# Kernel optimization log

Measured on AMD Instinct MI355X. Metric: run time of the kernel, lower is better.

Reference implementation:

```python
import jax, jax.numpy as jnp
import numpy as np

B, S, D = 16, 2048, 64
K, M = 8, 2048

def setup_inputs() -> dict:
    key = jax.random.key(0)
    kx, kc = jax.random.split(key)
    x = jax.random.normal(kx, (B, S, D), dtype=jnp.float32)
    # nn.init.uniform_(weight, -1/M, 1/M)
    codebooks = jax.random.uniform(kc, (K, M, D), dtype=jnp.float32,
                                   minval=-1.0 / M, maxval=1.0 / M)
    return {"x": x, "codebooks": codebooks}

def reference(x, codebooks):
    """Residual VQ: sequentially quantize residual against K codebooks.

    x: (B,S,D) float32; codebooks: (K,M,D) float32.
    Returns (quantized (B,S,D), indices (K,B,S) int32).
    Uses squared-distance expansion ||r||^2 - 2 r.c + ||c||^2 (argmin-equivalent
    to torch.norm) to avoid materializing the (B,S,M,D) difference tensor.
    """
    def step(residual, cb):  # residual: (B,S,D), cb: (M,D)
        r2 = jnp.sum(residual * residual, axis=-1, keepdims=True)   # (B,S,1)
        c2 = jnp.sum(cb * cb, axis=-1)                              # (M,)
        cross = jnp.einsum('bsd,md->bsm', residual, cb)             # (B,S,M)
        d2 = r2 - 2.0 * cross + c2                                  # (B,S,M)
        idx = jnp.argmin(d2, axis=-1)                               # (B,S)
        q = cb[idx]                                                 # (B,S,D) gather
        return residual - q, idx

    residual, indices = jax.lax.scan(step, x, codebooks)
    quantized = x - residual
    return quantized, indices
```

## Files before the change

### kernel.cpp

```cpp
#include <hip/hip_runtime.h>


#define BB 16
#define SS 2048
#define DD 64
#define KK 8
#define MM 2048
#define NPTS (BB * SS)
#define QSIZE (NPTS * DD)
#define WPB 8
#define MCHUNK (MM / WPB)

__global__ __launch_bounds__(256) void rvq_prep(const float* __restrict__ cb,
                                                float* __restrict__ c2) {
#pragma clang fp contract(off)
    int tid = blockIdx.x * 256 + threadIdx.x;
    const float* row = cb + (size_t)tid * DD;
    float r[8];
#pragma unroll
    for (int j = 0; j < 8; ++j) { float v = row[j]; r[j] = v * v; }
#pragma unroll
    for (int i = 8; i < DD; i += 8) {
#pragma unroll
        for (int j = 0; j < 8; ++j) { float v = row[i + j]; float t = v * v; r[j] += t; }
    }
    c2[tid] = ((r[0] + r[1]) + (r[2] + r[3])) + ((r[4] + r[5]) + (r[6] + r[7]));
}

#define R2K(A, B, C, E) \
    "v_pk_mul_f32 v[92:93], v[" A "], v[" A "]\n\t" \
    "v_pk_add_f32 v[80:81], v[80:81], v[92:93]\n\t" \
    "v_pk_mul_f32 v[92:93], v[" B "], v[" B "]\n\t" \
    "v_pk_add_f32 v[82:83], v[82:83], v[92:93]\n\t" \
    "v_pk_mul_f32 v[92:93], v[" C "], v[" C "]\n\t" \
    "v_pk_add_f32 v[84:85], v[84:85], v[92:93]\n\t" \
    "v_pk_mul_f32 v[92:93], v[" E "], v[" E "]\n\t" \
    "v_pk_add_f32 v[86:87], v[86:87], v[92:93]\n\t"

#define GRP(SA, SB, VA, VB) \
    "v_pk_mul_f32 v[84:85], s[" SA "], v[" VA "]\n\t" \
    "v_pk_mul_f32 v[86:87], s[" SB "], v[" VB "]\n\t" \
    "v_pk_add_f32 v[80:81], v[80:81], v[84:85]\n\t" \
    "v_pk_add_f32 v[82:83], v[82:83], v[86:87]\n\t"

__global__ __launch_bounds__(512, 4) void rvq_step(const float* __restrict__ res_in,
                                                   float* __restrict__ res_out,
                                                   const float* __restrict__ cbk,
                                                   const float* __restrict__ c2k,
                                                   float* __restrict__ idx_out) {
#pragma clang fp contract(off)
    const int tid = threadIdx.x;
    const int lane = tid & 63;
    const int wv = __builtin_amdgcn_readfirstlane(tid >> 6);
    const int point = blockIdx.x * 64 + lane;

    const int m0 = wv * MCHUNK;
    const float* cbw = cbk + (size_t)m0 * DD;
    const float* c2w = c2k + m0;
    const unsigned long long ra = (unsigned long long)(res_in + (size_t)point * DD);

    float best;
    int bidx;
    asm volatile(
        "global_load_dwordx4 v[16:19], %[ra], off\n\t"
        "global_load_dwordx4 v[20:23], %[ra], off offset:16\n\t"
        "global_load_dwordx4 v[24:27], %[ra], off offset:32\n\t"
        "global_load_dwordx4 v[28:31], %[ra], off offset:48\n\t"
        "global_load_dwordx4 v[32:35], %[ra], off offset:64\n\t"
        "global_load_dwordx4 v[36:39], %[ra], off offset:80\n\t"
        "global_load_dwordx4 v[40:43], %[ra], off offset:96\n\t"
        "global_load_dwordx4 v[44:47], %[ra], off offset:112\n\t"
        "global_load_dwordx4 v[48:51], %[ra], off offset:128\n\t"
        "global_load_dwordx4 v[52:55], %[ra], off offset:144\n\t"
        "global_load_dwordx4 v[56:59], %[ra], off offset:160\n\t"
        "global_load_dwordx4 v[60:63], %[ra], off offset:176\n\t"
        "global_load_dwordx4 v[64:67], %[ra], off offset:192\n\t"
        "global_load_dwordx4 v[68:71], %[ra], off offset:208\n\t"
        "global_load_dwordx4 v[72:75], %[ra], off offset:224\n\t"
        "global_load_dwordx4 v[76:79], %[ra], off offset:240\n\t"
        "s_waitcnt vmcnt(0)\n\t"
        "v_pk_mul_f32 v[80:81], v[16:17], v[16:17]\n\t"
        "v_pk_mul_f32 v[82:83], v[18:19], v[18:19]\n\t"
        "v_pk_mul_f32 v[84:85], v[20:21], v[20:21]\n\t"
        "v_pk_mul_f32 v[86:87], v[22:23], v[22:23]\n\t"
        R2K("24:25", "26:27", "28:29", "30:31")
        R2K("32:33", "34:35", "36:37", "38:39")
        R2K("40:41", "42:43", "44:45", "46:47")
        R2K("48:49", "50:51", "52:53", "54:55")
        R2K("56:57", "58:59", "60:61", "62:63")
        R2K("64:65", "66:67", "68:69", "70:71")
        R2K("72:73", "74:75", "76:77", "78:79")
        "v_add_f32 v92, v80, v81\n\t"
        "v_add_f32 v93, v82, v83\n\t"
        "v_add_f32 v92, v92, v93\n\t"
        "v_add_f32 v93, v84, v85\n\t"
        "v_add_f32 v88, v86, v87\n\t"
        "v_add_f32 v93, v93, v88\n\t"
        "v_add_f32 v88, v92, v93\n\t"
        "v_mov_b32 v89, 0x7f800000\n\t"
        "v_mov_b32 v90, 0\n\t"
        "s_mov_b32 s29, 0\n\t"
        "Lrvq_%=:\n\t"
        "s_load_dwordx16 s[32:47], %[cb], s29\n\t"
        "s_add_u32 s30, s29, 64\n\t"
        "s_load_dwordx16 s[48:63], %[cb], s30\n\t"
        "s_add_u32 s30, s29, 128\n\t"
        "s_load_dwordx16 s[64:79], %[cb], s30\n\t"
        "s_add_u32 s30, s29, 192\n\t"
        "s_load_dwordx16 s[80:95], %[cb], s30\n\t"
        "s_lshr_b32 s31, s29, 6\n\t"
        "s_load_dword s28, %[c2], s31\n\t"
        "s_lshr_b32 s30, s29, 8\n\t"
        "s_add_u32 s30, s30, %[m0]\n\t"
        "v_mov_b32 v91, s30\n\t"
        "s_waitcnt lgkmcnt(0)\n\t"
        "v_pk_mul_f32 v[80:81], s[44:45], v[28:29]\n\t"
        "v_pk_mul_f32 v[82:83], s[46:47], v[30:31]\n\t"
        GRP("40:41", "42:43", "24:25", "26:27")
        GRP("36:37", "38:39", "20:21", "22:23")
        GRP("32:33", "34:35", "16:17", "18:19")
        GRP("60:61", "62:63", "44:45", "46:47")
        GRP("56:57", "58:59", "40:41", "42:43")
        GRP("52:53", "54:55", "36:37", "38:39")
        GRP("48:49", "50:51", "32:33", "34:35")
        GRP("76:77", "78:79", "60:61", "62:63")
        GRP("72:73", "74:75", "56:57", "58:59")
        GRP("68:69", "70:71", "52:53", "54:55")
        GRP("64:65", "66:67", "48:49", "50:51")
        GRP("92:93", "94:95", "76:77", "78:79")
        GRP("88:89", "90:91", "72:73", "74:75")
        GRP("84:85", "86:87", "68:69", "70:71")
        GRP("80:81", "82:83", "64:65", "66:67")
        "v_add_f32 v92, v80, v81\n\t"
        "v_add_f32 v93, v82, v83\n\t"
        "v_add_f32 v92, v92, v93\n\t"
        "v_fma_f32 v92, v92, -2.0, v88\n\t"
        "v_add_f32 v92, s28, v92\n\t"
        "v_cmp_lt_f32 vcc, v92, v89\n\t"
        "v_cndmask_b32 v89, v89, v92, vcc\n\t"
        "v_cndmask_b32 v90, v90, v91, vcc\n\t"
        "s_add_u32 s29, s29, 256\n\t"
        "s_cmp_lg_u32 s29, 0x10000\n\t"
        "s_cbranch_scc1 Lrvq_%=\n\t"
        "v_mov_b32 %[ob], v89\n\t"
        "v_mov_b32 %[oi], v90\n\t"
        : [ob] "=v"(best), [oi] "=v"(bidx)
        : [ra] "v"(ra), [cb] "s"(cbw), [c2] "s"(c2w), [m0] "s"(m0)
        : "vcc", "scc",
          "v16","v17","v18","v19","v20","v21","v22","v23","v24","v25","v26","v27",
          "v28","v29","v30","v31","v32","v33","v34","v35","v36","v37","v38","v39",
          "v40","v41","v42","v43","v44","v45","v46","v47","v48","v49","v50","v51",
          "v52","v53","v54","v55","v56","v57","v58","v59","v60","v61","v62","v63",
          "v64","v65","v66","v67","v68","v69","v70","v71","v72","v73","v74","v75",
          "v76","v77","v78","v79","v80","v81","v82","v83","v84","v85","v86","v87",
          "v88","v89","v90","v91","v92","v93",
          "s28","s29","s30","s31","s32","s33","s34","s35","s36","s37","s38","s39",
          "s40","s41","s42","s43","s44","s45","s46","s47","s48","s49","s50","s51",
          "s52","s53","s54","s55","s56","s57","s58","s59","s60","s61","s62","s63",
          "s64","s65","s66","s67","s68","s69","s70","s71","s72","s73","s74","s75",
          "s76","s77","s78","s79","s80","s81","s82","s83","s84","s85","s86","s87",
          "s88","s89","s90","s91","s92","s93","s94","s95");

    __shared__ float sb[WPB * 64];
    __shared__ int   si[WPB * 64];
    __shared__ int   fidx[64];
    sb[wv * 64 + lane] = best;
    si[wv * 64 + lane] = bidx;
    __syncthreads();
    if (tid < 64) {
        float b = sb[lane];
        int ix = si[lane];
#pragma unroll
        for (int w = 1; w < WPB; ++w) {
            float ob = sb[w * 64 + lane];
            int oi = si[w * 64 + lane];
            if (ob < b) { b = ob; ix = oi; }
        }
        fidx[lane] = ix;
        idx_out[point] = (float)ix;
    }
    __syncthreads();

    const size_t base = (size_t)blockIdx.x * 64 * DD;
#pragma unroll
    for (int i = 0; i < 8; ++i) {
        const int e = i * 512 + tid;
        const int p = e >> 6;
        const int d = e & 63;
        const int ix = fidx[p];
        res_out[base + e] = res_in[base + e] - cbk[(size_t)ix * DD + d];
    }
}

__global__ __launch_bounds__(256) void rvq_final(const float* __restrict__ x,
                                                 const float* __restrict__ res,
                                                 float* __restrict__ q) {
#pragma clang fp contract(off)
    int i = blockIdx.x * 256 + threadIdx.x;
    q[i] = x[i] - res[i];
}

extern "C" void kernel_launch(void* const* d_in, const int* in_sizes, int n_in,
                              void* d_out, int out_size, void* d_ws, size_t ws_size,
                              hipStream_t stream) {
    const float* x  = (const float*)d_in[0];
    const float* cb = (const float*)d_in[1];

    float* out = (float*)d_out;
    float* quant = out;
    float* idx_out = out + QSIZE;

    float* c2   = (float*)d_ws;
    float* res1 = c2 + (size_t)KK * MM;
    float* R[2] = { quant, res1 };

    rvq_prep<<<(KK * MM) / 256, 256, 0, stream>>>(cb, c2);

    for (int k = 0; k < KK; ++k) {
        const float* rin = (k == 0) ? x : R[(k - 1) & 1];
        float* rout = R[k & 1];
        rvq_step<<<NPTS / 64, 512, 0, stream>>>(
            rin, rout,
            cb + (size_t)k * MM * DD,
            c2 + (size_t)k * MM,
            idx_out + (size_t)k * NPTS);
    }

    rvq_final<<<QSIZE / 256, 256, 0, stream>>>(x, R[(KK - 1) & 1], quant);
}
```

Before: 1.321 ms.

## Stream codebook rows via double-buffered vector loads instead of scalar loads

The codebook row for each distance step was read with scalar s_load_dwordx16 followed by a full lgkmcnt(0) wait. It is now read with wave-uniform global_load_dwordx4 into VGPRs, using two register buffers so the next row is in flight while the current one is computed. Waves per block drop from 8 to 4, so each wave scans 512 codes, and launch bounds change to 256 threads with 2 blocks per CU. The intent is to hide memory latency behind compute, at the cost of about 230 VGPRs and therefore lower occupancy. Every lane also loads the same address redundantly through the vector memory path.

```diff
diff --git a/kernel.cpp b/kernel.cpp
--- a/kernel.cpp
+++ b/kernel.cpp
@@ -8,7 +8,7 @@
 #define MM 2048
 #define NPTS (BB * SS)
 #define QSIZE (NPTS * DD)
-#define WPB 8
+#define WPB 4
 #define MCHUNK (MM / WPB)
 
 __global__ __launch_bounds__(256) void rvq_prep(const float* __restrict__ cb,
@@ -37,13 +37,100 @@
     "v_pk_mul_f32 v[92:93], v[" E "], v[" E "]\n\t" \
     "v_pk_add_f32 v[86:87], v[86:87], v[92:93]\n\t"
 
-#define GRP(SA, SB, VA, VB) \
-    "v_pk_mul_f32 v[84:85], s[" SA "], v[" VA "]\n\t" \
-    "v_pk_mul_f32 v[86:87], s[" SB "], v[" VB "]\n\t" \
+#define GRPV(CA, CB, RA, RB) \
+    "v_pk_mul_f32 v[84:85], v[" CA "], v[" RA "]\n\t" \
+    "v_pk_mul_f32 v[86:87], v[" CB "], v[" RB "]\n\t" \
     "v_pk_add_f32 v[80:81], v[80:81], v[84:85]\n\t" \
     "v_pk_add_f32 v[82:83], v[82:83], v[86:87]\n\t"
 
-__global__ __launch_bounds__(512, 4) void rvq_step(const float* __restrict__ res_in,
+#define LDA \
+    "global_load_dwordx4 v[96:99],   v94, %[cb]\n\t"            \
+    "global_load_dwordx4 v[100:103], v94, %[cb] offset:16\n\t"  \
+    "global_load_dwordx4 v[104:107], v94, %[cb] offset:32\n\t"  \
+    "global_load_dwordx4 v[108:111], v94, %[cb] offset:48\n\t"  \
+    "global_load_dwordx4 v[112:115], v94, %[cb] offset:64\n\t"  \
+    "global_load_dwordx4 v[116:119], v94, %[cb] offset:80\n\t"  \
+    "global_load_dwordx4 v[120:123], v94, %[cb] offset:96\n\t"  \
+    "global_load_dwordx4 v[124:127], v94, %[cb] offset:112\n\t" \
+    "global_load_dwordx4 v[128:131], v94, %[cb] offset:128\n\t" \
+    "global_load_dwordx4 v[132:135], v94, %[cb] offset:144\n\t" \
+    "global_load_dwordx4 v[136:139], v94, %[cb] offset:160\n\t" \
+    "global_load_dwordx4 v[140:143], v94, %[cb] offset:176\n\t" \
+    "global_load_dwordx4 v[144:147], v94, %[cb] offset:192\n\t" \
+    "global_load_dwordx4 v[148:151], v94, %[cb] offset:208\n\t" \
+    "global_load_dwordx4 v[152:155], v94, %[cb] offset:224\n\t" \
+    "global_load_dwordx4 v[156:159], v94, %[cb] offset:240\n\t" \
+    "global_load_dword   v160,       v95, %[c2]\n\t"
+
+#define LDB \
+    "global_load_dwordx4 v[164:167], v94, %[cb] offset:256\n\t" \
+    "global_load_dwordx4 v[168:171], v94, %[cb] offset:272\n\t" \
+    "global_load_dwordx4 v[172:175], v94, %[cb] offset:288\n\t" \
+    "global_load_dwordx4 v[176:179], v94, %[cb] offset:304\n\t" \
+    "global_load_dwordx4 v[180:183], v94, %[cb] offset:320\n\t" \
+    "global_load_dwordx4 v[184:187], v94, %[cb] offset:336\n\t" \
+    "global_load_dwordx4 v[188:191], v94, %[cb] offset:352\n\t" \
+    "global_load_dwordx4 v[192:195], v94, %[cb] offset:368\n\t" \
+    "global_load_dwordx4 v[196:199], v94, %[cb] offset:384\n\t" \
+    "global_load_dwordx4 v[200:203], v94, %[cb] offset:400\n\t" \
+    "global_load_dwordx4 v[204:207], v94, %[cb] offset:416\n\t" \
+    "global_load_dwordx4 v[208:211], v94, %[cb] offset:432\n\t" \
+    "global_load_dwordx4 v[212:215], v94, %[cb] offset:448\n\t" \
+    "global_load_dwordx4 v[216:219], v94, %[cb] offset:464\n\t" \
+    "global_load_dwordx4 v[220:223], v94, %[cb] offset:480\n\t" \
+    "global_load_dwordx4 v[224:227], v94, %[cb] offset:496\n\t" \
+    "global_load_dword   v228,       v95, %[c2] offset:4\n\t"
+
+#define EINA \
+    "v_pk_mul_f32 v[80:81], v[108:109], v[28:29]\n\t" \
+    "v_pk_mul_f32 v[82:83], v[110:111], v[30:31]\n\t" \
+    GRPV("104:105","106:107","24:25","26:27") \
+    GRPV("100:101","102:103","20:21","22:23") \
+    GRPV("96:97","98:99","16:17","18:19") \
+    GRPV("124:125","126:127","44:45","46:47") \
+    GRPV("120:121","122:123","40:41","42:43") \
+    GRPV("116:117","118:119","36:37","38:39") \
+    GRPV("112:113","114:115","32:33","34:35") \
+    GRPV("140:141","142:143","60:61","62:63") \
+    GRPV("136:137","138:139","56:57","58:59") \
+    GRPV("132:133","134:135","52:53","54:55") \
+    GRPV("128:129","130:131","48:49","50:51") \
+    GRPV("156:157","158:159","76:77","78:79") \
+    GRPV("152:153","154:155","72:73","74:75") \
+    GRPV("148:149","150:151","68:69","70:71") \
+    GRPV("144:145","146:147","64:65","66:67")
+
+#define EINB \
+    "v_pk_mul_f32 v[80:81], v[176:177], v[28:29]\n\t" \
+    "v_pk_mul_f32 v[82:83], v[178:179], v[30:31]\n\t" \
+    GRPV("172:173","174:175","24:25","26:27") \
+    GRPV("168:169","170:171","20:21","22:23") \
+    GRPV("164:165","166:167","16:17","18:19") \
+    GRPV("192:193","194:195","44:45","46:47") \
+    GRPV("188:189","190:191","40:41","42:43") \
+    GRPV("184:185","186:187","36:37","38:39") \
+    GRPV("180:181","182:183","32:33","34:35") \
+    GRPV("208:209","210:211","60:61","62:63") \
+    GRPV("204:205","206:207","56:57","58:59") \
+    GRPV("200:201","202:203","52:53","54:55") \
+    GRPV("196:197","198:199","48:49","50:51") \
+    GRPV("224:225","226:227","76:77","78:79") \
+    GRPV("220:221","222:223","72:73","74:75") \
+    GRPV("216:217","218:219","68:69","70:71") \
+    GRPV("212:213","214:215","64:65","66:67")
+
+#define FIN(C2) \
+    "v_add_f32 v92, v80, v81\n\t" \
+    "v_add_f32 v93, v82, v83\n\t" \
+    "v_add_f32 v92, v92, v93\n\t" \
+    "v_fma_f32 v92, v92, -2.0, v88\n\t" \
+    "v_add_f32 v92, v" C2 ", v92\n\t" \
+    "v_cmp_lt_f32 vcc, v92, v89\n\t" \
+    "v_cndmask_b32 v89, v89, v92, vcc\n\t" \
+    "v_cndmask_b32 v90, v90, v91, vcc\n\t" \
+    "v_add_u32 v91, 1, v91\n\t"
+
+__global__ __launch_bounds__(256, 2) void rvq_step(const float* __restrict__ res_in,
                                                    float* __restrict__ res_out,
                                                    const float* __restrict__ cbk,
                                                    const float* __restrict__ c2k,
@@ -99,67 +186,56 @@
         "v_add_f32 v88, v92, v93\n\t"
         "v_mov_b32 v89, 0x7f800000\n\t"
         "v_mov_b32 v90, 0\n\t"
+        "v_mov_b32 v91, %[m0]\n\t"
+        "v_mov_b32 v94, 0\n\t"
+        "v_mov_b32 v95, 0\n\t"
+        LDA
+        LDB
+        "v_mov_b32 v94, 0x200\n\t"
+        "v_mov_b32 v95, 8\n\t"
         "s_mov_b32 s29, 0\n\t"
         "Lrvq_%=:\n\t"
-        "s_load_dwordx16 s[32:47], %[cb], s29\n\t"
-        "s_add_u32 s30, s29, 64\n\t"
-        "s_load_dwordx16 s[48:63], %[cb], s30\n\t"
-        "s_add_u32 s30, s29, 128\n\t"
-        "s_load_dwordx16 s[64:79], %[cb], s30\n\t"
-        "s_add_u32 s30, s29, 192\n\t"
-        "s_load_dwordx16 s[80:95], %[cb], s30\n\t"
-        "s_lshr_b32 s31, s29, 6\n\t"
-        "s_load_dword s28, %[c2], s31\n\t"
-        "s_lshr_b32 s30, s29, 8\n\t"
-        "s_add_u32 s30, s30, %[m0]\n\t"
-        "v_mov_b32 v91, s30\n\t"
-        "s_waitcnt lgkmcnt(0)\n\t"
-        "v_pk_mul_f32 v[80:81], s[44:45], v[28:29]\n\t"
-        "v_pk_mul_f32 v[82:83], s[46:47], v[30:31]\n\t"
-        GRP("40:41", "42:43", "24:25", "26:27")
-        GRP("36:37", "38:39", "20:21", "22:23")
-        GRP("32:33", "34:35", "16:17", "18:19")
-        GRP("60:61", "62:63", "44:45", "46:47")
-        GRP("56:57", "58:59", "40:41", "42:43")
-        GRP("52:53", "54:55", "36:37", "38:39")
-        GRP("48:49", "50:51", "32:33", "34:35")
-        GRP("76:77", "78:79", "60:61", "62:63")
-        GRP("72:73", "74:75", "56:57", "58:59")
-        GRP("68:69", "70:71", "52:53", "54:55")
-        GRP("64:65", "66:67", "48:49", "50:51")
-        GRP("92:93", "94:95", "76:77", "78:79")
-        GRP("88:89", "90:91", "72:73", "74:75")
-        GRP("84:85", "86:87", "68:69", "70:71")
-        GRP("80:81", "82:83", "64:65", "66:67")
-        "v_add_f32 v92, v80, v81\n\t"
-        "v_add_f32 v93, v82, v83\n\t"
-        "v_add_f32 v92, v92, v93\n\t"
-        "v_fma_f32 v92, v92, -2.0, v88\n\t"
-        "v_add_f32 v92, s28, v92\n\t"
-        "v_cmp_lt_f32 vcc, v92, v89\n\t"
-        "v_cndmask_b32 v89, v89, v92, vcc\n\t"
-        "v_cndmask_b32 v90, v90, v91, vcc\n\t"
-        "s_add_u32 s29, s29, 256\n\t"
-        "s_cmp_lg_u32 s29, 0x10000\n\t"
+        "s_waitcnt vmcnt(17)\n\t"
+        EINA
+        FIN("160")
+        LDA
+        "s_waitcnt vmcnt(17)\n\t"
+        EINB
+        FIN("228")
+        LDB
+        "v_add_u32 v94, 0x200, v94\n\t"
+        "v_min_u32 v94, 0x1fe00, v94\n\t"
+        "v_add_u32 v95, 8, v95\n\t"
+        "v_min_u32 v95, 0x7f8, v95\n\t"
+        "s_add_u32 s29, s29, 1\n\t"
+        "s_cmp_lg_u32 s29, 256\n\t"
         "s_cbranch_scc1 Lrvq_%=\n\t"
+        "s_waitcnt vmcnt(0)\n\t"
         "v_mov_b32 %[ob], v89\n\t"
         "v_mov_b32 %[oi], v90\n\t"
         : [ob] "=v"(best), [oi] "=v"(bidx)
         : [ra] "v"(ra), [cb] "s"(cbw), [c2] "s"(c2w), [m0] "s"(m0)
-        : "vcc", "scc",
+        : "vcc", "scc", "s29",
           "v16","v17","v18","v19","v20","v21","v22","v23","v24","v25","v26","v27",
           "v28","v29","v30","v31","v32","v33","v34","v35","v36","v37","v38","v39",
           "v40","v41","v42","v43","v44","v45","v46","v47","v48","v49","v50","v51",
           "v52","v53","v54","v55","v56","v57","v58","v59","v60","v61","v62","v63",
           "v64","v65","v66","v67","v68","v69","v70","v71","v72","v73","v74","v75",
           "v76","v77","v78","v79","v80","v81","v82","v83","v84","v85","v86","v87",
-          "v88","v89","v90","v91","v92","v93",
-          "s28","s29","s30","s31","s32","s33","s34","s35","s36","s37","s38","s39",
-          "s40","s41","s42","s43","s44","s45","s46","s47","s48","s49","s50","s51",
-          "s52","s53","s54","s55","s56","s57","s58","s59","s60","s61","s62","s63",
-          "s64","s65","s66","s67","s68","s69","s70","s71","s72","s73","s74","s75",
-          "s76","s77","s78","s79","s80","s81","s82","s83","s84","s85","s86","s87",
-          "s88","s89","s90","s91","s92","s93","s94","s95");
+          "v88","v89","v90","v91","v92","v93","v94","v95","v96","v97","v98","v99",
+          "v100","v101","v102","v103","v104","v105","v106","v107","v108","v109",
+          "v110","v111","v112","v113","v114","v115","v116","v117","v118","v119",
+          "v120","v121","v122","v123","v124","v125","v126","v127","v128","v129",
+          "v130","v131","v132","v133","v134","v135","v136","v137","v138","v139",
+          "v140","v141","v142","v143","v144","v145","v146","v147","v148","v149",
+          "v150","v151","v152","v153","v154","v155","v156","v157","v158","v159",
+          "v160","v161","v162","v163","v164","v165","v166","v167","v168","v169",
+          "v170","v171","v172","v173","v174","v175","v176","v177","v178","v179",
+          "v180","v181","v182","v183","v184","v185","v186","v187","v188","v189",
+          "v190","v191","v192","v193","v194","v195","v196","v197","v198","v199",
+          "v200","v201","v202","v203","v204","v205","v206","v207","v208","v209",
+          "v210","v211","v212","v213","v214","v215","v216","v217","v218","v219",
+          "v220","v221","v222","v223","v224","v225","v226","v227","v228");
 
     __shared__ float sb[WPB * 64];
     __shared__ int   si[WPB * 64];
@@ -183,8 +259,8 @@
 
     const size_t base = (size_t)blockIdx.x * 64 * DD;
 #pragma unroll
-    for (int i = 0; i < 8; ++i) {
-        const int e = i * 512 + tid;
+    for (int i = 0; i < 16; ++i) {
+        const int e = i * 256 + tid;
         const int p = e >> 6;
         const int d = e & 63;
         const int ix = fidx[p];
@@ -219,7 +295,7 @@
     for (int k = 0; k < KK; ++k) {
         const float* rin = (k == 0) ? x : R[(k - 1) & 1];
         float* rout = R[k & 1];
-        rvq_step<<<NPTS / 64, 512, 0, stream>>>(
+        rvq_step<<<NPTS / 64, 256, 0, stream>>>(
             rin, rout,
             cb + (size_t)k * MM * DD,
             c2 + (size_t)k * MM,
```

New measurement: 3.742 ms. 183% more time.

## Process 128 points per block with paired waves sharing codebook chunks

Applied to the files above, without the earlier changes.

Each block now handles 128 points using 1024 threads: 16 waves form 8 codebook chunks, with two waves (covering two 64-point halves) per chunk. The intent is to let two waves reuse the same scalar-loaded codebook chunk, and to halve the number of blocks and the per-block reduction overhead. The cost is larger blocks, which may limit occupancy scheduling, and more contention on scalar cache loads. Launch bounds of 1024 with a minimum of 4 blocks may also strain register allocation.

```diff
diff --git a/kernel.cpp b/kernel.cpp
--- a/kernel.cpp
+++ b/kernel.cpp
@@ -8,8 +8,10 @@
 #define MM 2048
 #define NPTS (BB * SS)
 #define QSIZE (NPTS * DD)
-#define WPB 8
-#define MCHUNK (MM / WPB)
+#define WPB 16
+#define NCHUNK 8
+#define PPB 128
+#define MCHUNK (MM / NCHUNK)
 
 __global__ __launch_bounds__(256) void rvq_prep(const float* __restrict__ cb,
                                                 float* __restrict__ c2) {
@@ -43,18 +45,20 @@
     "v_pk_add_f32 v[80:81], v[80:81], v[84:85]\n\t" \
     "v_pk_add_f32 v[82:83], v[82:83], v[86:87]\n\t"
 
-__global__ __launch_bounds__(512, 4) void rvq_step(const float* __restrict__ res_in,
-                                                   float* __restrict__ res_out,
-                                                   const float* __restrict__ cbk,
-                                                   const float* __restrict__ c2k,
-                                                   float* __restrict__ idx_out) {
+__global__ __launch_bounds__(1024, 4) void rvq_step(const float* __restrict__ res_in,
+                                                    float* __restrict__ res_out,
+                                                    const float* __restrict__ cbk,
+                                                    const float* __restrict__ c2k,
+                                                    float* __restrict__ idx_out) {
 #pragma clang fp contract(off)
     const int tid = threadIdx.x;
     const int lane = tid & 63;
     const int wv = __builtin_amdgcn_readfirstlane(tid >> 6);
-    const int point = blockIdx.x * 64 + lane;
-
-    const int m0 = wv * MCHUNK;
+    const int ch = wv >> 1;
+    const int hf = wv & 1;
+    const int point = blockIdx.x * PPB + hf * 64 + lane;
+
+    const int m0 = ch * MCHUNK;
     const float* cbw = cbk + (size_t)m0 * DD;
     const float* c2w = c2k + m0;
     const unsigned long long ra = (unsigned long long)(res_in + (size_t)point * DD);
@@ -163,28 +167,31 @@
 
     __shared__ float sb[WPB * 64];
     __shared__ int   si[WPB * 64];
-    __shared__ int   fidx[64];
+    __shared__ int   fidx[PPB];
     sb[wv * 64 + lane] = best;
     si[wv * 64 + lane] = bidx;
     __syncthreads();
-    if (tid < 64) {
-        float b = sb[lane];
-        int ix = si[lane];
-#pragma unroll
-        for (int w = 1; w < WPB; ++w) {
-            float ob = sb[w * 64 + lane];
-            int oi = si[w * 64 + lane];
+    if (tid < PPB) {
+        const int h = tid >> 6;
+        const int l = tid & 63;
+        float b = sb[h * 64 + l];
+        int ix = si[h * 64 + l];
+#pragma unroll
+        for (int c = 1; c < NCHUNK; ++c) {
+            const int w = c * 2 + h;
+            float ob = sb[w * 64 + l];
+            int oi = si[w * 64 + l];
             if (ob < b) { b = ob; ix = oi; }
         }
-        fidx[lane] = ix;
-        idx_out[point] = (float)ix;
+        fidx[tid] = ix;
+        idx_out[blockIdx.x * PPB + tid] = (float)ix;
     }
     __syncthreads();
 
-    const size_t base = (size_t)blockIdx.x * 64 * DD;
+    const size_t base = (size_t)blockIdx.x * PPB * DD;
 #pragma unroll
     for (int i = 0; i < 8; ++i) {
-        const int e = i * 512 + tid;
+        const int e = i * 1024 + tid;
         const int p = e >> 6;
         const int d = e & 63;
         const int ix = fidx[p];
@@ -219,7 +226,7 @@
     for (int k = 0; k < KK; ++k) {
         const float* rin = (k == 0) ? x : R[(k - 1) & 1];
         float* rout = R[k & 1];
-        rvq_step<<<NPTS / 64, 512, 0, stream>>>(
+        rvq_step<<<NPTS / PPB, 1024, 0, stream>>>(
             rin, rout,
             cb + (size_t)k * MM * DD,
             c2 + (size_t)k * MM,
```

New measurement: 1.410 ms. 6.8% more time.

## Split codebook search across blocks with atomicMin argmin and separate update kernel

Applied to the files above, without the earlier changes.

The codebook is now split across 8 blocks per group of 512 points. In each block all 8 waves scan the same codebook chunk for different points, with periodic barriers so the waves stay in step and share scalar-cache codebook loads. Per-chunk results are merged across blocks by a 64-bit atomicMin on a packed (distance bits, index) key, replacing the shared-memory reduction. A separate update kernel then reads the winners, resets the keys, writes indices, subtracts the codeword and on the last step folds in the final x - residual. This adds a kernel launch per step plus global atomics, and the packed float ordering is only correct when the distances are non-negative.

```diff
diff --git a/kernel.cpp b/kernel.cpp
--- a/kernel.cpp
+++ b/kernel.cpp
@@ -8,11 +8,14 @@
 #define MM 2048
 #define NPTS (BB * SS)
 #define QSIZE (NPTS * DD)
+#define NCHUNK 8
 #define WPB 8
-#define MCHUNK (MM / WPB)
+#define PPB 512
+#define MCHUNK (MM / NCHUNK)
 
 __global__ __launch_bounds__(256) void rvq_prep(const float* __restrict__ cb,
-                                                float* __restrict__ c2) {
+                                                float* __restrict__ c2,
+                                                unsigned long long* __restrict__ keys) {
 #pragma clang fp contract(off)
     int tid = blockIdx.x * 256 + threadIdx.x;
     const float* row = cb + (size_t)tid * DD;
@@ -25,6 +28,8 @@
         for (int j = 0; j < 8; ++j) { float v = row[i + j]; float t = v * v; r[j] += t; }
     }
     c2[tid] = ((r[0] + r[1]) + (r[2] + r[3])) + ((r[4] + r[5]) + (r[6] + r[7]));
+    keys[tid] = ~0ULL;
+    keys[tid + KK * MM] = ~0ULL;
 }
 
 #define R2K(A, B, C, E) \
@@ -43,18 +48,19 @@
     "v_pk_add_f32 v[80:81], v[80:81], v[84:85]\n\t" \
     "v_pk_add_f32 v[82:83], v[82:83], v[86:87]\n\t"
 
-__global__ __launch_bounds__(512, 4) void rvq_step(const float* __restrict__ res_in,
-                                                   float* __restrict__ res_out,
+__global__ __launch_bounds__(512, 4) void rvq_main(const float* __restrict__ res_in,
                                                    const float* __restrict__ cbk,
                                                    const float* __restrict__ c2k,
-                                                   float* __restrict__ idx_out) {
+                                                   unsigned long long* __restrict__ keys) {
 #pragma clang fp contract(off)
     const int tid = threadIdx.x;
     const int lane = tid & 63;
     const int wv = __builtin_amdgcn_readfirstlane(tid >> 6);
-    const int point = blockIdx.x * 64 + lane;
-
-    const int m0 = wv * MCHUNK;
+    const int ch = blockIdx.x & (NCHUNK - 1);
+    const int bp = blockIdx.x >> 3;
+    const int point = bp * PPB + wv * 64 + lane;
+
+    const int m0 = ch * MCHUNK;
     const float* cbw = cbk + (size_t)m0 * DD;
     const float* c2w = c2k + m0;
     const unsigned long long ra = (unsigned long long)(res_in + (size_t)point * DD);
@@ -101,6 +107,11 @@
         "v_mov_b32 v90, 0\n\t"
         "s_mov_b32 s29, 0\n\t"
         "Lrvq_%=:\n\t"
+        "s_and_b32 s30, s29, 0x7ff\n\t"
+        "s_cmp_lg_u32 s30, 0\n\t"
+        "s_cbranch_scc1 Lnb_%=\n\t"
+        "s_barrier\n\t"
+        "Lnb_%=:\n\t"
         "s_load_dwordx16 s[32:47], %[cb], s29\n\t"
         "s_add_u32 s30, s29, 64\n\t"
         "s_load_dwordx16 s[48:63], %[cb], s30\n\t"
@@ -161,43 +172,36 @@
           "s76","s77","s78","s79","s80","s81","s82","s83","s84","s85","s86","s87",
           "s88","s89","s90","s91","s92","s93","s94","s95");
 
-    __shared__ float sb[WPB * 64];
-    __shared__ int   si[WPB * 64];
-    __shared__ int   fidx[64];
-    sb[wv * 64 + lane] = best;
-    si[wv * 64 + lane] = bidx;
-    __syncthreads();
-    if (tid < 64) {
-        float b = sb[lane];
-        int ix = si[lane];
-#pragma unroll
-        for (int w = 1; w < WPB; ++w) {
-            float ob = sb[w * 64 + lane];
-            int oi = si[w * 64 + lane];
-            if (ob < b) { b = ob; ix = oi; }
-        }
-        fidx[lane] = ix;
-        idx_out[point] = (float)ix;
+    unsigned long long key =
+        ((unsigned long long)__float_as_uint(best) << 32) | (unsigned int)bidx;
+    atomicMin(&keys[point], key);
+}
+
+__global__ __launch_bounds__(256) void rvq_update(const float* __restrict__ res_in,
+                                                  float* __restrict__ res_out,
+                                                  const float* __restrict__ x,
+                                                  const float* __restrict__ cbk,
+                                                  unsigned long long* __restrict__ keys,
+                                                  float* __restrict__ idx_out,
+                                                  int last) {
+#pragma clang fp contract(off)
+    __shared__ unsigned long long sk[4];
+    const int tid = threadIdx.x;
+    const int e = blockIdx.x * 256 + tid;
+    const int p0 = blockIdx.x * 4;
+    if (tid < 4) {
+        unsigned long long k = keys[p0 + tid];
+        sk[tid] = k;
+        keys[p0 + tid] = ~0ULL;
+        idx_out[p0 + tid] = (float)(unsigned int)k;
     }
     __syncthreads();
-
-    const size_t base = (size_t)blockIdx.x * 64 * DD;
-#pragma unroll
-    for (int i = 0; i < 8; ++i) {
-        const int e = i * 512 + tid;
-        const int p = e >> 6;
-        const int d = e & 63;
-        const int ix = fidx[p];
-        res_out[base + e] = res_in[base + e] - cbk[(size_t)ix * DD + d];
-    }
-}
-
-__global__ __launch_bounds__(256) void rvq_final(const float* __restrict__ x,
-                                                 const float* __restrict__ res,
-                                                 float* __restrict__ q) {
-#pragma clang fp contract(off)
-    int i = blockIdx.x * 256 + threadIdx.x;
-    q[i] = x[i] - res[i];
+    const int pi = tid >> 6;
+    const int d = tid & 63;
+    const int m = (int)(unsigned int)sk[pi];
+    const float r = res_in[e] - cbk[(size_t)m * DD + d];
+    if (last) res_out[e] = x[e] - r;
+    else      res_out[e] = r;
 }
 
 extern "C" void kernel_launch(void* const* d_in, const int* in_sizes, int n_in,
@@ -212,19 +216,26 @@
 
     float* c2   = (float*)d_ws;
     float* res1 = c2 + (size_t)KK * MM;
+    unsigned long long* keys =
+        (unsigned long long*)(res1 + (size_t)QSIZE);
     float* R[2] = { quant, res1 };
 
-    rvq_prep<<<(KK * MM) / 256, 256, 0, stream>>>(cb, c2);
+    rvq_prep<<<(KK * MM) / 256, 256, 0, stream>>>(cb, c2, keys);
 
     for (int k = 0; k < KK; ++k) {
         const float* rin = (k == 0) ? x : R[(k - 1) & 1];
-        float* rout = R[k & 1];
-        rvq_step<<<NPTS / 64, 512, 0, stream>>>(
-            rin, rout,
+        const int last = (k == KK - 1);
+        float* rout = last ? quant : R[k & 1];
+        rvq_main<<<(NPTS / PPB) * NCHUNK, PPB, 0, stream>>>(
+            rin,
             cb + (size_t)k * MM * DD,
             c2 + (size_t)k * MM,
-            idx_out + (size_t)k * NPTS);
+            keys);
+        rvq_update<<<QSIZE / 256, 256, 0, stream>>>(
+            rin, rout, x,
+            cb + (size_t)k * MM * DD,
+            keys,
+            idx_out + (size_t)k * NPTS,
+            last);
     }
-
-    rvq_final<<<QSIZE / 256, 256, 0, stream>>>(x, R[(KK - 1) & 1], quant);
-}
+}
```

Measured after the change: 1.350 ms. 1.02x slower.
